# Kernel tuning notes

Measured on AMD Instinct MI355X. Metric: run time of the kernel, lower is better.

Reference implementation:

```python
import jax, jax.numpy as jnp
import numpy as np

N_NODES = 100000
N_EDGES = 1600000
HID = 64


def setup_inputs() -> dict:
    key = jax.random.key(0)
    ks = jax.random.split(key, 16)
    s = 0.05
    inp = {
        "x": jax.random.normal(ks[0], (N_NODES, HID), dtype=jnp.float32),
        "edge_index": jax.random.randint(ks[1], (2, N_EDGES), 0, N_NODES, dtype=jnp.int32),
        # GatedGraphConv (num_layers=1): weight shape [out, out], used as x @ W
        "W_conv": jax.random.normal(ks[2], (HID, HID), dtype=jnp.float32) * s,
        # torch.nn.GRUCell params (gate order: r, z, n)
        "gru_w_ih": jax.random.normal(ks[3], (3 * HID, HID), dtype=jnp.float32) * s,
        "gru_w_hh": jax.random.normal(ks[4], (3 * HID, HID), dtype=jnp.float32) * s,
        "gru_b_ih": jax.random.normal(ks[5], (3 * HID,), dtype=jnp.float32) * s,
        "gru_b_hh": jax.random.normal(ks[6], (3 * HID,), dtype=jnp.float32) * s,
        # torch.nn.LSTM single layer params (gate order: i, f, g, o)
        "lstm_w_ih": jax.random.normal(ks[7], (4 * HID, HID), dtype=jnp.float32) * s,
        "lstm_w_hh": jax.random.normal(ks[8], (4 * HID, HID), dtype=jnp.float32) * s,
        "lstm_b_ih": jax.random.normal(ks[9], (4 * HID,), dtype=jnp.float32) * s,
        "lstm_b_hh": jax.random.normal(ks[10], (4 * HID,), dtype=jnp.float32) * s,
        # output Linear(hidden, hidden)
        "lin_w": jax.random.normal(ks[11], (HID, HID), dtype=jnp.float32) * s,
        "lin_b": jax.random.normal(ks[12], (HID,), dtype=jnp.float32) * s,
    }
    return inp


def _sigmoid(v):
    return jax.nn.sigmoid(v)


def reference(x, edge_index, W_conv, gru_w_ih, gru_w_hh, gru_b_ih, gru_b_hh,
              lstm_w_ih, lstm_w_hh, lstm_b_ih, lstm_b_hh, lin_w, lin_b):
    N = x.shape[0]
    H = W_conv.shape[0]
    # --- GatedGraphConv(out=H, num_layers=1, aggr='mean') ---
    # pad features to out_channels if needed (no-op here since input_dim == H)
    if x.shape[1] < H:
        x = jnp.pad(x, ((0, 0), (0, H - x.shape[1])))
    m = x @ W_conv                                    # [N, H]
    src, dst = edge_index[0], edge_index[1]
    # mean aggregation of source messages at destination nodes
    agg = jax.ops.segment_sum(m[src], dst, num_segments=N)          # [N, H]
    cnt = jax.ops.segment_sum(jnp.ones_like(src, dtype=m.dtype), dst, num_segments=N)
    agg = agg / jnp.maximum(cnt, 1.0)[:, None]
    # GRUCell(agg, x): gates r, z, n
    gi = agg @ gru_w_ih.T + gru_b_ih                  # [N, 3H]
    gh = x @ gru_w_hh.T + gru_b_hh                    # [N, 3H]
    ir, iz, inn = jnp.split(gi, 3, axis=1)
    hr, hz, hn = jnp.split(gh, 3, axis=1)
    r = _sigmoid(ir + hr)
    z = _sigmoid(iz + hz)
    n = jnp.tanh(inn + r * hn)
    h_conv = (1.0 - z) * n + z * x                    # [N, H]
    # --- LSTM (1 layer, seq_len=1, zero initial (H, C)) ---
    gates = h_conv @ lstm_w_ih.T + lstm_b_ih + lstm_b_hh   # h0 = 0 -> W_hh @ h0 = 0
    gi_, gf_, gg_, go_ = jnp.split(gates, 4, axis=1)
    c = _sigmoid(gi_) * jnp.tanh(gg_)                 # f * c0 = 0
    h_tilde = _sigmoid(go_) * jnp.tanh(c)             # [N, H]
    # --- ReLU + Linear ---
    out = jax.nn.relu(h_tilde) @ lin_w.T + lin_b      # [N, H]
    return out
```

## Files before the change

kernel.cpp:

```cpp
#include <hip/hip_runtime.h>
#include <math.h>

#define N_NODES 100000
#define N_EDGES 1600000
#define PAD_DEG 64

typedef __bf16 bf16_t;
typedef __attribute__((ext_vector_type(8))) __bf16 bf16x8;
typedef __attribute__((ext_vector_type(4))) __bf16 bf16x4;
typedef __attribute__((ext_vector_type(4))) float f32x4;

#define GT_WHH  0
#define GT_WIH  12
#define GT_LSTM 24
#define GT_LIN  36
#define N_GT    40
#define PACK_ELEMS (N_GT * 1024)
#define CAST_BLOCKS ((N_NODES * 16 + 16 + 255) / 256)
#define PACK_BLOCKS ((PACK_ELEMS + 255) / 256)

#define NODES_PER_RANGE 12500
#define PLACE_GROUP 304
#define PLACE_BLOCKS (8 * PLACE_GROUP)

__device__ __forceinline__ float sigm(float v) { return 1.f / (1.f + __expf(-v)); }
__device__ __forceinline__ float tanh_(float v) { return 2.f * sigm(2.f * v) - 1.f; }

__device__ __forceinline__ void split8(const float* __restrict__ p, bf16x8& hi, bf16x8& lo) {
    f32x4 a = *(const f32x4*)p;
    f32x4 b = *(const f32x4*)(p + 4);
#pragma unroll
    for (int i = 0; i < 4; ++i) {
        float v = a[i];
        __bf16 h = (__bf16)v;
        hi[i] = h;
        lo[i] = (__bf16)(v - (float)h);
        v = b[i];
        h = (__bf16)v;
        hi[4 + i] = h;
        lo[4 + i] = (__bf16)(v - (float)h);
    }
}

__device__ __forceinline__ bf16x8 zero8() {
    bf16x8 r;
#pragma unroll
    for (int i = 0; i < 8; ++i) r[i] = (__bf16)0.f;
    return r;
}

__device__ __forceinline__ f32x4 mm6(f32x4 acc, bf16x8 ah0, bf16x8 ah1, bf16x8 al0, bf16x8 al1,
                                     const bf16_t* __restrict__ ph, const bf16_t* __restrict__ pl,
                                     int gt, int l) {
    const bf16x8 bh0 = *(const bf16x8*)(ph + (gt * 2 + 0) * 512 + l * 8);
    const bf16x8 bh1 = *(const bf16x8*)(ph + (gt * 2 + 1) * 512 + l * 8);
    const bf16x8 bl0 = *(const bf16x8*)(pl + (gt * 2 + 0) * 512 + l * 8);
    const bf16x8 bl1 = *(const bf16x8*)(pl + (gt * 2 + 1) * 512 + l * 8);
    acc = __builtin_amdgcn_mfma_f32_16x16x32_bf16(ah0, bh0, acc, 0, 0, 0);
    acc = __builtin_amdgcn_mfma_f32_16x16x32_bf16(ah1, bh1, acc, 0, 0, 0);
    acc = __builtin_amdgcn_mfma_f32_16x16x32_bf16(al0, bh0, acc, 0, 0, 0);
    acc = __builtin_amdgcn_mfma_f32_16x16x32_bf16(al1, bh1, acc, 0, 0, 0);
    acc = __builtin_amdgcn_mfma_f32_16x16x32_bf16(ah0, bl0, acc, 0, 0, 0);
    acc = __builtin_amdgcn_mfma_f32_16x16x32_bf16(ah1, bl1, acc, 0, 0, 0);
    return acc;
}

__global__ __launch_bounds__(256) void k_pre(const float* __restrict__ x, bf16_t* __restrict__ xb,
                                             const float* __restrict__ Wc,
                                             const float* __restrict__ wih,
                                             const float* __restrict__ whh,
                                             const float* __restrict__ lw,
                                             const float* __restrict__ lin,
                                             bf16_t* __restrict__ ph, bf16_t* __restrict__ pl,
                                             const int* __restrict__ ei,
                                             int* __restrict__ cnt, int* __restrict__ ss) {
    int b = blockIdx.x;
    if (b < CAST_BLOCKS) {
        int t = b * 256 + threadIdx.x;
        if (t < N_NODES * 16) {
            f32x4 v = *(const f32x4*)(x + (size_t)t * 4);
            bf16x4 o;
#pragma unroll
            for (int i = 0; i < 4; ++i) o[i] = (__bf16)v[i];
            *(bf16x4*)(xb + (size_t)t * 4) = o;
        } else if (t < N_NODES * 16 + 16) {
            bf16x4 o;
#pragma unroll
            for (int i = 0; i < 4; ++i) o[i] = (__bf16)0.f;
            *(bf16x4*)(xb + (size_t)t * 4) = o;
        }
        return;
    }
    b -= CAST_BLOCKS;
    if (b < PACK_BLOCKS) {
        int t = b * 256 + threadIdx.x;
        if (t >= PACK_ELEMS) return;
        int i = t & 7, lane = (t >> 3) & 63, kk = (t >> 9) & 1, gt = t >> 10;
        int f = lane & 15;
        int k = kk * 32 + (lane >> 4) * 8 + i;
        float v;
        if (gt < 12) {
            v = whh[(gt * 16 + f) * 64 + k];
        } else if (gt < 24) {
            int j = (gt - 12) * 16 + f;
            float acc = 0.f;
            for (int c = 0; c < 64; ++c) acc += Wc[k * 64 + c] * wih[j * 64 + c];
            v = acc;
        } else if (gt < 36) {
            int jg = (gt - 24) * 16 + f;
            int row = (jg < 64) ? jg : jg + 64;
            v = lw[row * 64 + k];
        } else {
            v = lin[((gt - 36) * 16 + f) * 64 + k];
        }
        __bf16 h = (__bf16)v;
        ph[t] = h;
        pl[t] = (__bf16)(v - (float)h);
        return;
    }
    b -= PACK_BLOCKS;
    int r = b & 7, gi = b >> 3;
    int lo = r * NODES_PER_RANGE;
    int hi = lo + NODES_PER_RANGE;
    for (int e = gi * 256 + threadIdx.x; e < N_EDGES; e += PLACE_GROUP * 256) {
        int d = ei[N_EDGES + e];
        if (d >= lo && d < hi) {
            int s = ei[e];
            int p = atomicAdd(&cnt[d], 1);
            if (p < PAD_DEG) ss[d * PAD_DEG + p] = s;
        }
    }
}

__global__ __launch_bounds__(256) void k_fused(
    const float* __restrict__ x, const bf16_t* __restrict__ xb,
    const int* __restrict__ ss, const int* __restrict__ cnt,
    const bf16_t* __restrict__ ph, const bf16_t* __restrict__ pl,
    const float* __restrict__ b_ih, const float* __restrict__ b_hh,
    const float* __restrict__ lb_ih, const float* __restrict__ lb_hh,
    const float* __restrict__ lin_b, float* __restrict__ out) {
    __shared__ float sc[4 * 16 * 68];
    int tid = threadIdx.x, w = tid >> 6, l = tid & 63;
    int base = blockIdx.x * 64 + w * 16;
    float* sw = &sc[w * 16 * 68];
    int f16 = l & 15, k0 = (l >> 4) * 8, hq = l >> 4;
    int g8 = l >> 3, f8 = (l & 7) * 8;

    int dcl = 0;
    if (l < 16 && base + l < N_NODES) dcl = cnt[base + l];
    if (dcl > PAD_DEG) dcl = PAD_DEG;

    int idxq = 0;
    if (base < N_NODES) idxq = ss[(size_t)base * PAD_DEG + l];

#pragma unroll 1
    for (int t = 0; t < 16; ++t) {
        int dc = __shfl(dcl, t, 64);
        int idxv = (l < dc) ? idxq : N_NODES;
        if (t < 15 && base + t + 1 < N_NODES) idxq = ss[(size_t)(base + t + 1) * PAD_DEG + l];
        float a[8];
#pragma unroll
        for (int c = 0; c < 8; ++c) a[c] = 0.f;
        int nst = (dc + 7) >> 3;
        for (int st = 0; st < nst; st += 2) {
            int en0 = st * 8 + g8;
            int en1 = en0 + 8;
            int s0 = __shfl(idxv, en0, 64);
            int s1 = __shfl(idxv, en1, 64);
            bf16x8 v0 = *(const bf16x8*)(xb + (size_t)s0 * 64 + f8);
            bf16x8 v1 = *(const bf16x8*)(xb + (size_t)s1 * 64 + f8);
#pragma unroll
            for (int c = 0; c < 8; ++c) a[c] += (float)v0[c] + (float)v1[c];
        }
#pragma unroll
        for (int c = 0; c < 8; ++c) {
            a[c] += __shfl_xor(a[c], 8, 64);
            a[c] += __shfl_xor(a[c], 16, 64);
            a[c] += __shfl_xor(a[c], 32, 64);
        }
        float inv = 1.f / fmaxf((float)dc, 1.f);
        if (l < 8) {
            f32x4 o0 = {a[0] * inv, a[1] * inv, a[2] * inv, a[3] * inv};
            f32x4 o1 = {a[4] * inv, a[5] * inv, a[6] * inv, a[7] * inv};
            *(f32x4*)&sw[t * 68 + f8] = o0;
            *(f32x4*)&sw[t * 68 + f8 + 4] = o1;
        }
    }

    bf16x8 ah0, al0, ah1, al1;
    split8(&sw[f16 * 68 + k0], ah0, al0);
    split8(&sw[f16 * 68 + 32 + k0], ah1, al1);

    bf16x8 xh0 = zero8(), xl0 = zero8(), xh1 = zero8(), xl1 = zero8();
    {
        int xrow = base + f16;
        if (xrow < N_NODES) {
            split8(&x[xrow * 64 + k0], xh0, xl0);
            split8(&x[xrow * 64 + 32 + k0], xh1, xl1);
        }
    }

#pragma unroll 1
    for (int jj = 0; jj < 4; ++jj) {
        float bhr = b_hh[jj * 16 + f16], bhz = b_hh[64 + jj * 16 + f16], bhn = b_hh[128 + jj * 16 + f16];
        f32x4 ghr = {bhr, bhr, bhr, bhr}, ghz = {bhz, bhz, bhz, bhz}, ghn = {bhn, bhn, bhn, bhn};
        ghr = mm6(ghr, xh0, xh1, xl0, xl1, ph, pl, GT_WHH + jj, l);
        ghz = mm6(ghz, xh0, xh1, xl0, xl1, ph, pl, GT_WHH + 4 + jj, l);
        ghn = mm6(ghn, xh0, xh1, xl0, xl1, ph, pl, GT_WHH + 8 + jj, l);
        __builtin_amdgcn_sched_barrier(0);
        float bir = b_ih[jj * 16 + f16], biz = b_ih[64 + jj * 16 + f16], bin_ = b_ih[128 + jj * 16 + f16];
        f32x4 gir = {bir, bir, bir, bir}, giz = {biz, biz, biz, biz}, gin = {bin_, bin_, bin_, bin_};
        gir = mm6(gir, ah0, ah1, al0, al1, ph, pl, GT_WIH + jj, l);
        giz = mm6(giz, ah0, ah1, al0, al1, ph, pl, GT_WIH + 4 + jj, l);
        gin = mm6(gin, ah0, ah1, al0, al1, ph, pl, GT_WIH + 8 + jj, l);
        __builtin_amdgcn_sched_barrier(0);
#pragma unroll
        for (int rr = 0; rr < 4; ++rr) {
            int row = base + hq * 4 + rr;
            float xc = (row < N_NODES) ? x[row * 64 + jj * 16 + f16] : 0.f;
            float gr = sigm(gir[rr] + ghr[rr]);
            float gz = sigm(giz[rr] + ghz[rr]);
            float gn = tanh_(gin[rr] + gr * ghn[rr]);
            sw[(hq * 4 + rr) * 68 + jj * 16 + f16] = (1.f - gz) * gn + gz * xc;
        }
    }

    bf16x8 hh0, hl0, hh1, hl1;
    split8(&sw[f16 * 68 + k0], hh0, hl0);
    split8(&sw[f16 * 68 + 32 + k0], hh1, hl1);

#pragma unroll 1
    for (int jj = 0; jj < 4; ++jj) {
        float bi = lb_ih[jj * 16 + f16] + lb_hh[jj * 16 + f16];
        float bg = lb_ih[128 + jj * 16 + f16] + lb_hh[128 + jj * 16 + f16];
        float bo = lb_ih[192 + jj * 16 + f16] + lb_hh[192 + jj * 16 + f16];
        f32x4 ai = {bi, bi, bi, bi}, ag = {bg, bg, bg, bg}, ao = {bo, bo, bo, bo};
        ai = mm6(ai, hh0, hh1, hl0, hl1, ph, pl, GT_LSTM + jj, l);
        ag = mm6(ag, hh0, hh1, hl0, hl1, ph, pl, GT_LSTM + 4 + jj, l);
        ao = mm6(ao, hh0, hh1, hl0, hl1, ph, pl, GT_LSTM + 8 + jj, l);
        __builtin_amdgcn_sched_barrier(0);
#pragma unroll
        for (int rr = 0; rr < 4; ++rr) {
            float c = sigm(ai[rr]) * tanh_(ag[rr]);
            float ht = sigm(ao[rr]) * tanh_(c);
            sw[(hq * 4 + rr) * 68 + jj * 16 + f16] = fmaxf(ht, 0.f);
        }
    }

    bf16x8 rh0, rl0, rh1, rl1;
    split8(&sw[f16 * 68 + k0], rh0, rl0);
    split8(&sw[f16 * 68 + 32 + k0], rh1, rl1);

#pragma unroll 1
    for (int jj = 0; jj < 4; ++jj) {
        float bb = lin_b[jj * 16 + f16];
        f32x4 acc = {bb, bb, bb, bb};
        acc = mm6(acc, rh0, rh1, rl0, rl1, ph, pl, GT_LIN + jj, l);
#pragma unroll
        for (int rr = 0; rr < 4; ++rr) {
            int row = base + hq * 4 + rr;
            if (row < N_NODES) __builtin_nontemporal_store(acc[rr], &out[row * 64 + jj * 16 + f16]);
        }
    }
}

extern "C" void kernel_launch(void* const* d_in, const int* in_sizes, int n_in,
                              void* d_out, int out_size, void* d_ws, size_t ws_size,
                              hipStream_t stream) {
    const float* x    = (const float*)d_in[0];
    const int*   ei   = (const int*)d_in[1];
    const float* Wc   = (const float*)d_in[2];
    const float* gwih = (const float*)d_in[3];
    const float* gwhh = (const float*)d_in[4];
    const float* gbih = (const float*)d_in[5];
    const float* gbhh = (const float*)d_in[6];
    const float* lwih = (const float*)d_in[7];
    const float* lbih = (const float*)d_in[9];
    const float* lbhh = (const float*)d_in[10];
    const float* linw = (const float*)d_in[11];
    const float* linb = (const float*)d_in[12];
    float* out = (float*)d_out;

    int*    ss  = (int*)d_ws;
    int*    cnt = ss + (size_t)N_NODES * PAD_DEG;
    bf16_t* ph  = (bf16_t*)(cnt + N_NODES);
    bf16_t* pl  = ph + PACK_ELEMS;
    bf16_t* xb  = pl + PACK_ELEMS;

    hipMemsetAsync(cnt, 0, (size_t)N_NODES * sizeof(int), stream);

    dim3 b(256);
    k_pre<<<dim3(CAST_BLOCKS + PACK_BLOCKS + PLACE_BLOCKS), b, 0, stream>>>(
        x, xb, Wc, gwih, gwhh, lwih, linw, ph, pl, ei, cnt, ss);
    k_fused<<<dim3((N_NODES + 63) / 64), b, 0, stream>>>(
        x, xb, ss, cnt, ph, pl, gbih, gbhh, lbih, lbhh, linb, out);
}
```

Baseline: 186.8 us.

## Restructure neighbor gather with fixed-unrolled loads and reorder pre-kernel block roles

The mean-aggregation gather now assigns 16 lanes per neighbor row with 4 features each and issues 4 or 8 independent row loads before accumulating, so more memory requests are in flight per wave. Nodes with at most 16 neighbors take a fixed 16-slot path; padded slots read the zero row. The pre-kernel also puts the atomic edge-placement blocks first so this long-running scatter starts earliest and overlaps with the cast and pack blocks. In exchange it issues extra loads for low-degree nodes, uses narrower 8-byte loads, and needs more registers.

```diff
diff --git a/kernel.cpp b/kernel.cpp
--- a/kernel.cpp
+++ b/kernel.cpp
@@ -75,6 +75,21 @@
                                              const int* __restrict__ ei,
                                              int* __restrict__ cnt, int* __restrict__ ss) {
     int b = blockIdx.x;
+    if (b < PLACE_BLOCKS) {
+        int r = b & 7, gi = b >> 3;
+        int lo = r * NODES_PER_RANGE;
+        int hi = lo + NODES_PER_RANGE;
+        for (int e = gi * 256 + threadIdx.x; e < N_EDGES; e += PLACE_GROUP * 256) {
+            int d = ei[N_EDGES + e];
+            if (d >= lo && d < hi) {
+                int s = ei[e];
+                int p = atomicAdd(&cnt[d], 1);
+                if (p < PAD_DEG) ss[d * PAD_DEG + p] = s;
+            }
+        }
+        return;
+    }
+    b -= PLACE_BLOCKS;
     if (b < CAST_BLOCKS) {
         int t = b * 256 + threadIdx.x;
         if (t < N_NODES * 16) {
@@ -92,44 +107,29 @@
         return;
     }
     b -= CAST_BLOCKS;
-    if (b < PACK_BLOCKS) {
-        int t = b * 256 + threadIdx.x;
-        if (t >= PACK_ELEMS) return;
-        int i = t & 7, lane = (t >> 3) & 63, kk = (t >> 9) & 1, gt = t >> 10;
-        int f = lane & 15;
-        int k = kk * 32 + (lane >> 4) * 8 + i;
-        float v;
-        if (gt < 12) {
-            v = whh[(gt * 16 + f) * 64 + k];
-        } else if (gt < 24) {
-            int j = (gt - 12) * 16 + f;
-            float acc = 0.f;
-            for (int c = 0; c < 64; ++c) acc += Wc[k * 64 + c] * wih[j * 64 + c];
-            v = acc;
-        } else if (gt < 36) {
-            int jg = (gt - 24) * 16 + f;
-            int row = (jg < 64) ? jg : jg + 64;
-            v = lw[row * 64 + k];
-        } else {
-            v = lin[((gt - 36) * 16 + f) * 64 + k];
-        }
-        __bf16 h = (__bf16)v;
-        ph[t] = h;
-        pl[t] = (__bf16)(v - (float)h);
-        return;
-    }
-    b -= PACK_BLOCKS;
-    int r = b & 7, gi = b >> 3;
-    int lo = r * NODES_PER_RANGE;
-    int hi = lo + NODES_PER_RANGE;
-    for (int e = gi * 256 + threadIdx.x; e < N_EDGES; e += PLACE_GROUP * 256) {
-        int d = ei[N_EDGES + e];
-        if (d >= lo && d < hi) {
-            int s = ei[e];
-            int p = atomicAdd(&cnt[d], 1);
-            if (p < PAD_DEG) ss[d * PAD_DEG + p] = s;
-        }
-    }
+    int t = b * 256 + threadIdx.x;
+    if (t >= PACK_ELEMS) return;
+    int i = t & 7, lane = (t >> 3) & 63, kk = (t >> 9) & 1, gt = t >> 10;
+    int f = lane & 15;
+    int k = kk * 32 + (lane >> 4) * 8 + i;
+    float v;
+    if (gt < 12) {
+        v = whh[(gt * 16 + f) * 64 + k];
+    } else if (gt < 24) {
+        int j = (gt - 12) * 16 + f;
+        float acc = 0.f;
+        for (int c = 0; c < 64; ++c) acc += Wc[k * 64 + c] * wih[j * 64 + c];
+        v = acc;
+    } else if (gt < 36) {
+        int jg = (gt - 24) * 16 + f;
+        int row = (jg < 64) ? jg : jg + 64;
+        v = lw[row * 64 + k];
+    } else {
+        v = lin[((gt - 36) * 16 + f) * 64 + k];
+    }
+    __bf16 h = (__bf16)v;
+    ph[t] = h;
+    pl[t] = (__bf16)(v - (float)h);
 }
 
 __global__ __launch_bounds__(256) void k_fused(
@@ -144,8 +144,9 @@
     int base = blockIdx.x * 64 + w * 16;
     float* sw = &sc[w * 16 * 68];
     int f16 = l & 15, k0 = (l >> 4) * 8, hq = l >> 4;
-    int g8 = l >> 3, f8 = (l & 7) * 8;
-
+
+    int g = l >> 4;
+    int f4 = (l & 15) * 4;
     int dcl = 0;
     if (l < 16 && base + l < N_NODES) dcl = cnt[base + l];
     if (dcl > PAD_DEG) dcl = PAD_DEG;
@@ -158,32 +159,40 @@
         int dc = __shfl(dcl, t, 64);
         int idxv = (l < dc) ? idxq : N_NODES;
         if (t < 15 && base + t + 1 < N_NODES) idxq = ss[(size_t)(base + t + 1) * PAD_DEG + l];
-        float a[8];
-#pragma unroll
-        for (int c = 0; c < 8; ++c) a[c] = 0.f;
-        int nst = (dc + 7) >> 3;
-        for (int st = 0; st < nst; st += 2) {
-            int en0 = st * 8 + g8;
-            int en1 = en0 + 8;
-            int s0 = __shfl(idxv, en0, 64);
-            int s1 = __shfl(idxv, en1, 64);
-            bf16x8 v0 = *(const bf16x8*)(xb + (size_t)s0 * 64 + f8);
-            bf16x8 v1 = *(const bf16x8*)(xb + (size_t)s1 * 64 + f8);
-#pragma unroll
-            for (int c = 0; c < 8; ++c) a[c] += (float)v0[c] + (float)v1[c];
-        }
-#pragma unroll
-        for (int c = 0; c < 8; ++c) {
-            a[c] += __shfl_xor(a[c], 8, 64);
-            a[c] += __shfl_xor(a[c], 16, 64);
-            a[c] += __shfl_xor(a[c], 32, 64);
-        }
+        float a0 = 0.f, a1 = 0.f, a2 = 0.f, a3 = 0.f;
+
+#define GLD(name, sb) \
+        int s##name = __shfl(idxv, (sb) + g, 64); \
+        bf16x4 v##name = *(const bf16x4*)(xb + (size_t)s##name * 64 + f4);
+#define GACC(name) \
+        a0 += (float)v##name[0]; a1 += (float)v##name[1]; \
+        a2 += (float)v##name[2]; a3 += (float)v##name[3];
+
+        if (dc <= 16) {
+            GLD(A, 0) GLD(B, 4) GLD(C, 8) GLD(D, 12)
+            GACC(A) GACC(B) GACC(C) GACC(D)
+        } else {
+            GLD(A, 0) GLD(B, 4) GLD(C, 8) GLD(D, 12)
+            GLD(E, 16) GLD(F, 20) GLD(G, 24) GLD(H, 28)
+            GACC(A) GACC(B) GACC(C) GACC(D)
+            GACC(E) GACC(F) GACC(G) GACC(H)
+            for (int e = 32 + g; e < dc; e += 4) {
+                int s_ = __shfl(idxv, e, 64);
+                bf16x4 v_ = *(const bf16x4*)(xb + (size_t)s_ * 64 + f4);
+                a0 += (float)v_[0]; a1 += (float)v_[1];
+                a2 += (float)v_[2]; a3 += (float)v_[3];
+            }
+        }
+#undef GLD
+#undef GACC
+        a0 += __shfl_xor(a0, 16, 64); a0 += __shfl_xor(a0, 32, 64);
+        a1 += __shfl_xor(a1, 16, 64); a1 += __shfl_xor(a1, 32, 64);
+        a2 += __shfl_xor(a2, 16, 64); a2 += __shfl_xor(a2, 32, 64);
+        a3 += __shfl_xor(a3, 16, 64); a3 += __shfl_xor(a3, 32, 64);
         float inv = 1.f / fmaxf((float)dc, 1.f);
-        if (l < 8) {
-            f32x4 o0 = {a[0] * inv, a[1] * inv, a[2] * inv, a[3] * inv};
-            f32x4 o1 = {a[4] * inv, a[5] * inv, a[6] * inv, a[7] * inv};
-            *(f32x4*)&sw[t * 68 + f8] = o0;
-            *(f32x4*)&sw[t * 68 + f8 + 4] = o1;
+        if (l < 16) {
+            f32x4 o = {a0 * inv, a1 * inv, a2 * inv, a3 * inv};
+            *(f32x4*)&sw[t * 68 + f4] = o;
         }
     }
 
@@ -290,7 +299,7 @@
     hipMemsetAsync(cnt, 0, (size_t)N_NODES * sizeof(int), stream);
 
     dim3 b(256);
-    k_pre<<<dim3(CAST_BLOCKS + PACK_BLOCKS + PLACE_BLOCKS), b, 0, stream>>>(
+    k_pre<<<dim3(PLACE_BLOCKS + CAST_BLOCKS + PACK_BLOCKS), b, 0, stream>>>(
         x, xb, Wc, gwih, gwhh, lwih, linw, ph, pl, ei, cnt, ss);
     k_fused<<<dim3((N_NODES + 63) / 64), b, 0, stream>>>(
         x, xb, ss, cnt, ph, pl, gbih, gbhh, lbih, lbhh, linb, out);
```

Measured after the change: 174.7 us. 1.07x faster.
